# Optimization experiments

Measured on AMD Instinct MI355X. Metric: run time of the kernel, lower is better.

Reference implementation:

```python
import jax, jax.numpy as jnp
import numpy as np

N_NODES = 100000
N_EDGES = 1600000
IN_FEATS = 128
OUT_FEATS = 256
K = 32


def setup_inputs() -> dict:
    key = jax.random.key(0)
    ks = jax.random.split(key, 8)
    feat = jax.random.normal(ks[0], (N_NODES, IN_FEATS), dtype=jnp.float32)
    # MaxK sparsified activations: nonnegative values (post-ReLU top-k)
    topk_values = jax.random.uniform(ks[1], (N_NODES, K), dtype=jnp.float32)
    topk_indices = jax.random.randint(ks[2], (N_NODES, K), 0, IN_FEATS, dtype=jnp.int32)
    # CSR expanded to COO: sorted row ids emulate indptr ordering
    row = jnp.sort(jax.random.randint(ks[3], (N_EDGES,), 0, N_NODES, dtype=jnp.int32))
    col = jax.random.randint(ks[4], (N_EDGES,), 0, N_NODES, dtype=jnp.int32)
    # in-degrees clamped to min 1.0, as in set_graph_data
    deg = jax.ops.segment_sum(jnp.ones((N_EDGES,), jnp.float32), row, num_segments=N_NODES)
    degrees = jnp.maximum(deg, 1.0)
    gain = float(np.sqrt(2.0))  # calculate_gain('relu')
    bnd_n = gain * np.sqrt(6.0 / (IN_FEATS + OUT_FEATS))
    W_neigh = jax.random.uniform(ks[5], (IN_FEATS, OUT_FEATS), jnp.float32, -bnd_n, bnd_n)
    W_self = jax.random.uniform(ks[6], (IN_FEATS, OUT_FEATS), jnp.float32, -bnd_n, bnd_n)
    bnd_b = 1.0 / np.sqrt(IN_FEATS)
    b_self = jax.random.uniform(ks[7], (OUT_FEATS,), jnp.float32, -bnd_b, bnd_b)
    return {"feat": feat, "topk_values": topk_values, "topk_indices": topk_indices,
            "row": row, "col": col, "degrees": degrees,
            "W_neigh": W_neigh, "W_self": W_self, "b_self": b_self}


def reference(feat, topk_values, topk_indices, row, col, degrees, W_neigh, W_self, b_self):
    n = feat.shape[0]
    # Scatter top-k sparse features back to dense [N, in_feats]
    # (real top-k indices are unique per row, so add == set; add is deterministic)
    rows = jnp.arange(n, dtype=jnp.int32)[:, None]
    x_sparse = jnp.zeros((n, IN_FEATS), feat.dtype).at[rows, topk_indices].add(topk_values)
    # CSR SpMM with all-ones edge values + degree normalization (mean aggregation)
    gathered = x_sparse[col]                                  # [E, in_feats]
    agg = jax.ops.segment_sum(gathered, row, num_segments=n)  # [N, in_feats]
    agg = agg / degrees[:, None]
    # lin_before_mp is False (in_feats <= out_feats): linear after aggregation
    h_neigh = agg @ W_neigh                                    # [N, out_feats]
    rst = feat @ W_self + b_self + h_neigh
    return rst
```

## Files before the change

### kernel.cpp

```cpp
#include <hip/hip_runtime.h>
#include <stdint.h>

#define IN_FEATS 128
#define OUT_FEATS 256
#define TOPK 32
#define BM 128
#define BN 128
#define BK 64
#define KTOT 256

typedef float f32x4 __attribute__((ext_vector_type(4)));
typedef short bf16x8 __attribute__((ext_vector_type(8)));

__device__ __forceinline__ unsigned short f2bf(float x) {
    unsigned u = __float_as_uint(x);
    u += 0x7FFFu + ((u >> 16) & 1u);
    return (unsigned short)(u >> 16);
}

__device__ __forceinline__ void gload16(const void* g, void* l) {
    __builtin_amdgcn_global_load_lds(
        (const __attribute__((address_space(1))) unsigned*)g,
        (__attribute__((address_space(3))) unsigned*)l, 16, 0, 0);
}

__global__ __launch_bounds__(256) void k_scatter(
    const float* __restrict__ vals, const int* __restrict__ idxs,
    const float* __restrict__ feat,
    unsigned short* __restrict__ xsp, unsigned short* __restrict__ Acat,
    int n_nodes) {
    __shared__ float lds[4 * IN_FEATS];
    int t = threadIdx.x;
    int n0 = blockIdx.x * 4;
    lds[t] = 0.f;
    lds[t + 256] = 0.f;
    __syncthreads();
    if (t < 4 * TOPK) {
        int h = t >> 5;
        int k = t & 31;
        int n = n0 + h;
        if (n < n_nodes) {
            float v = vals[(size_t)n * TOPK + k];
            int ix = idxs[(size_t)n * TOPK + k] & 127;
            atomicAdd(&lds[h * IN_FEATS + ix], v);
        }
    }
    __syncthreads();
    int h2 = t >> 6;
    int f2 = (t & 63) * 2;
    int n = n0 + h2;
    if (n < n_nodes) {
        unsigned lo = f2bf(lds[h2 * IN_FEATS + f2]);
        unsigned hi = f2bf(lds[h2 * IN_FEATS + f2 + 1]);
        *(unsigned*)(xsp + (size_t)n * IN_FEATS + f2) = lo | (hi << 16);
        float2 fv = *(const float2*)(feat + (size_t)n * IN_FEATS + f2);
        unsigned pk = (unsigned)f2bf(fv.x) | ((unsigned)f2bf(fv.y) << 16);
        *(unsigned*)(Acat + (size_t)n * KTOT + IN_FEATS + f2) = pk;
    }
}

__global__ void k_weights(const float* __restrict__ Wn, const float* __restrict__ Ws,
                          unsigned short* __restrict__ WT) {
    int idx = blockIdx.x * 256 + threadIdx.x;
    int n = idx >> 8;
    int k = idx & 255;
    float v = (k < IN_FEATS) ? Wn[(size_t)k * OUT_FEATS + n]
                             : Ws[(size_t)(k - IN_FEATS) * OUT_FEATS + n];
    WT[idx] = f2bf(v);
}

__global__ void k_indptr(const int* __restrict__ row, int* __restrict__ indptr,
                         int n_nodes, int n_edges) {
    int e = blockIdx.x * 256 + threadIdx.x;
    if (e >= n_edges) return;
    int r = row[e];
    int rp = (e == 0) ? -1 : row[e - 1];
    for (int x = rp + 1; x <= r; ++x) indptr[x] = e;
    if (e == n_edges - 1)
        for (int x = r + 1; x <= n_nodes; ++x) indptr[x] = n_edges;
}

__global__ __launch_bounds__(256) void k_aggregate(
    const unsigned short* __restrict__ xsp,
    const int* __restrict__ indptr, const int* __restrict__ col,
    unsigned short* __restrict__ Acat, int n_nodes) {
    int t = threadIdx.x;
    int node = blockIdx.x * 4 + (t >> 6);
    if (node >= n_nodes) return;
    int lane = t & 63;
    int eg = lane >> 4, fi = lane & 15;
    int e0 = indptr[node], e1 = indptr[node + 1];

    float acc[8] = {0.f, 0.f, 0.f, 0.f, 0.f, 0.f, 0.f, 0.f};
    int elast = (e1 > e0) ? (e1 - 1) : e0;
    for (int base = e0; base < e1; base += 16) {
        float s[4];
        int c[4];
        uint4 u[4];
#pragma unroll
        for (int j = 0; j < 4; ++j) {
            int ee = base + j * 4 + eg;
            s[j] = (ee < e1) ? 1.f : 0.f;
            c[j] = col[ee < elast ? ee : elast];
        }
#pragma unroll
        for (int j = 0; j < 4; ++j)
            u[j] = *(const uint4*)(xsp + (size_t)c[j] * IN_FEATS + fi * 8);
#pragma unroll
        for (int j = 0; j < 4; ++j) {
            unsigned p[4] = {u[j].x, u[j].y, u[j].z, u[j].w};
#pragma unroll
            for (int i = 0; i < 4; ++i) {
                acc[2 * i]     = fmaf(s[j], __uint_as_float(p[i] << 16), acc[2 * i]);
                acc[2 * i + 1] = fmaf(s[j], __uint_as_float(p[i] & 0xFFFF0000u), acc[2 * i + 1]);
            }
        }
    }
#pragma unroll
    for (int i = 0; i < 8; ++i) {
        acc[i] += __shfl_down(acc[i], 16, 64);
        acc[i] += __shfl_down(acc[i], 32, 64);
    }
    if (eg == 0) {
        int cnt = e1 - e0;
        float inv = 1.0f / (float)(cnt > 0 ? cnt : 1);
        unsigned o[4];
#pragma unroll
        for (int i = 0; i < 4; ++i) {
            unsigned lo = f2bf(acc[2 * i] * inv);
            unsigned hi = f2bf(acc[2 * i + 1] * inv);
            o[i] = lo | (hi << 16);
        }
        *(uint4*)(Acat + (size_t)node * KTOT + fi * 8) = *(uint4*)&o[0];
    }
}

__global__ __launch_bounds__(256) void k_gemm(
    const unsigned short* __restrict__ Acat,
    const unsigned short* __restrict__ WT,
    const float* __restrict__ bias,
    float* __restrict__ out, int n_nodes) {
    __shared__ __align__(16) unsigned short Ash[BM * BK];
    __shared__ __align__(16) unsigned short Bsh[BN * BK];
    int t = threadIdx.x;
    int m0 = blockIdx.x * BM;
    int n0 = blockIdx.y * BN;
    int lane = t & 63;
    int w = t >> 6;
    int wr = w >> 1, wc = w & 1;
    int lrow = lane & 15, quad = lane >> 4;

    f32x4 acc[4][4];
#pragma unroll
    for (int i = 0; i < 4; ++i)
#pragma unroll
        for (int j = 0; j < 4; ++j)
            acc[i][j] = (f32x4){0.f, 0.f, 0.f, 0.f};

    for (int kk = 0; kk < KTOT; kk += BK) {
#pragma unroll
        for (int p = 0; p < 4; ++p) {
            int c = p * 256 + t;
            int row = c >> 3;
            int q = (c & 7) ^ (row & 7);
            int nodeA = m0 + row;
            if (nodeA >= n_nodes) nodeA = n_nodes - 1;
            gload16(Acat + (size_t)nodeA * KTOT + kk + q * 8, &Ash[(size_t)c * 8]);
            gload16(WT + (size_t)(n0 + row) * KTOT + kk + q * 8, &Bsh[(size_t)c * 8]);
        }
        __syncthreads();

#pragma unroll
        for (int ks = 0; ks < 2; ++ks) {
            bf16x8 af[4], bfr[4];
#pragma unroll
            for (int mi = 0; mi < 4; ++mi) {
                int r = wr * 64 + mi * 16 + lrow;
                int q = (ks * 4 + quad) ^ (r & 7);
                af[mi] = *(const bf16x8*)&Ash[(r * 8 + q) * 8];
            }
#pragma unroll
            for (int ni = 0; ni < 4; ++ni) {
                int r = wc * 64 + ni * 16 + lrow;
                int q = (ks * 4 + quad) ^ (r & 7);
                bfr[ni] = *(const bf16x8*)&Bsh[(r * 8 + q) * 8];
            }
#pragma unroll
            for (int mi = 0; mi < 4; ++mi)
#pragma unroll
                for (int ni = 0; ni < 4; ++ni)
                    acc[mi][ni] = __builtin_amdgcn_mfma_f32_16x16x32_bf16(
                        af[mi], bfr[ni], acc[mi][ni], 0, 0, 0);
        }
        __syncthreads();
    }

#pragma unroll
    for (int mi = 0; mi < 4; ++mi) {
        int gm = m0 + wr * 64 + mi * 16 + quad * 4;
#pragma unroll
        for (int ni = 0; ni < 4; ++ni) {
            int go = n0 + wc * 64 + ni * 16 + lrow;
            float b = bias[go];
#pragma unroll
            for (int r = 0; r < 4; ++r) {
                int node = gm + r;
                if (node < n_nodes)
                    out[(size_t)node * OUT_FEATS + go] = acc[mi][ni][r] + b;
            }
        }
    }
}

extern "C" void kernel_launch(void* const* d_in, const int* in_sizes, int n_in,
                              void* d_out, int out_size, void* d_ws, size_t ws_size,
                              hipStream_t stream) {
    const float* feat = (const float*)d_in[0];
    const float* tkv  = (const float*)d_in[1];
    const int*   tki  = (const int*)d_in[2];
    const int*   row  = (const int*)d_in[3];
    const int*   col  = (const int*)d_in[4];
    const float* Wn   = (const float*)d_in[6];
    const float* Ws   = (const float*)d_in[7];
    const float* bias = (const float*)d_in[8];
    float* out = (float*)d_out;

    int n_nodes = in_sizes[5];
    int n_edges = in_sizes[3];

    unsigned short* xsp  = (unsigned short*)d_ws;
    unsigned short* Acat = xsp + (size_t)n_nodes * IN_FEATS;
    unsigned short* WT   = Acat + (size_t)n_nodes * KTOT;
    int* indptr = (int*)(WT + (size_t)OUT_FEATS * KTOT);

    k_scatter<<<(n_nodes + 3) / 4, 256, 0, stream>>>(tkv, tki, feat, xsp, Acat, n_nodes);
    k_weights<<<256, 256, 0, stream>>>(Wn, Ws, WT);
    k_indptr<<<(n_edges + 255) / 256, 256, 0, stream>>>(row, indptr, n_nodes, n_edges);
    k_aggregate<<<(n_nodes + 3) / 4, 256, 0, stream>>>(xsp, indptr, col, Acat, n_nodes);
    dim3 g3((n_nodes + BM - 1) / BM, OUT_FEATS / BN);
    k_gemm<<<g3, 256, 0, stream>>>(Acat, WT, bias, out, n_nodes);
}
```

Measured before the change: 289.4 us.

## Drop indptr kernel via binary search and widen GEMM tile to full N

Removes the separate indptr-construction kernel. Each wavefront in the aggregate kernel now finds its CSR edge range with two binary searches over the sorted row array. The GEMM now uses 512-thread blocks that cover all 256 output columns, so each A tile is loaded once instead of twice. The cost is about 17 dependent global loads per node for the searches, plus higher LDS use and register pressure per GEMM block, which may lower occupancy.

```diff
diff --git a/kernel.cpp b/kernel.cpp
--- a/kernel.cpp
+++ b/kernel.cpp
@@ -5,7 +5,7 @@
 #define OUT_FEATS 256
 #define TOPK 32
 #define BM 128
-#define BN 128
+#define BN 256
 #define BK 64
 #define KTOT 256
 
@@ -69,27 +69,22 @@
     WT[idx] = f2bf(v);
 }
 
-__global__ void k_indptr(const int* __restrict__ row, int* __restrict__ indptr,
-                         int n_nodes, int n_edges) {
-    int e = blockIdx.x * 256 + threadIdx.x;
-    if (e >= n_edges) return;
-    int r = row[e];
-    int rp = (e == 0) ? -1 : row[e - 1];
-    for (int x = rp + 1; x <= r; ++x) indptr[x] = e;
-    if (e == n_edges - 1)
-        for (int x = r + 1; x <= n_nodes; ++x) indptr[x] = n_edges;
-}
-
 __global__ __launch_bounds__(256) void k_aggregate(
     const unsigned short* __restrict__ xsp,
-    const int* __restrict__ indptr, const int* __restrict__ col,
-    unsigned short* __restrict__ Acat, int n_nodes) {
+    const int* __restrict__ row, const int* __restrict__ col,
+    unsigned short* __restrict__ Acat, int n_nodes, int n_edges) {
     int t = threadIdx.x;
     int node = blockIdx.x * 4 + (t >> 6);
     if (node >= n_nodes) return;
     int lane = t & 63;
     int eg = lane >> 4, fi = lane & 15;
-    int e0 = indptr[node], e1 = indptr[node + 1];
+
+    int lo = 0, hi = n_edges;
+    while (lo < hi) { int mid = (lo + hi) >> 1; if (row[mid] < node) lo = mid + 1; else hi = mid; }
+    int e0 = lo;
+    hi = n_edges;
+    while (lo < hi) { int mid = (lo + hi) >> 1; if (row[mid] <= node) lo = mid + 1; else hi = mid; }
+    int e1 = lo;
 
     float acc[8] = {0.f, 0.f, 0.f, 0.f, 0.f, 0.f, 0.f, 0.f};
     int elast = (e1 > e0) ? (e1 - 1) : e0;
@@ -127,15 +122,15 @@
         unsigned o[4];
 #pragma unroll
         for (int i = 0; i < 4; ++i) {
-            unsigned lo = f2bf(acc[2 * i] * inv);
-            unsigned hi = f2bf(acc[2 * i + 1] * inv);
-            o[i] = lo | (hi << 16);
+            unsigned lo2 = f2bf(acc[2 * i] * inv);
+            unsigned hi2 = f2bf(acc[2 * i + 1] * inv);
+            o[i] = lo2 | (hi2 << 16);
         }
         *(uint4*)(Acat + (size_t)node * KTOT + fi * 8) = *(uint4*)&o[0];
     }
 }
 
-__global__ __launch_bounds__(256) void k_gemm(
+__global__ __launch_bounds__(512) void k_gemm(
     const unsigned short* __restrict__ Acat,
     const unsigned short* __restrict__ WT,
     const float* __restrict__ bias,
@@ -144,10 +139,9 @@
     __shared__ __align__(16) unsigned short Bsh[BN * BK];
     int t = threadIdx.x;
     int m0 = blockIdx.x * BM;
-    int n0 = blockIdx.y * BN;
     int lane = t & 63;
     int w = t >> 6;
-    int wr = w >> 1, wc = w & 1;
+    int wr = w >> 2, wc = w & 3;
     int lrow = lane & 15, quad = lane >> 4;
 
     f32x4 acc[4][4];
@@ -159,14 +153,20 @@
 
     for (int kk = 0; kk < KTOT; kk += BK) {
 #pragma unroll
-        for (int p = 0; p < 4; ++p) {
-            int c = p * 256 + t;
-            int row = c >> 3;
-            int q = (c & 7) ^ (row & 7);
-            int nodeA = m0 + row;
+        for (int p = 0; p < 2; ++p) {
+            int c = p * 512 + t;
+            int rowi = c >> 3;
+            int q = (c & 7) ^ (rowi & 7);
+            int nodeA = m0 + rowi;
             if (nodeA >= n_nodes) nodeA = n_nodes - 1;
             gload16(Acat + (size_t)nodeA * KTOT + kk + q * 8, &Ash[(size_t)c * 8]);
-            gload16(WT + (size_t)(n0 + row) * KTOT + kk + q * 8, &Bsh[(size_t)c * 8]);
+        }
+#pragma unroll
+        for (int p = 0; p < 4; ++p) {
+            int c = p * 512 + t;
+            int rowi = c >> 3;
+            int q = (c & 7) ^ (rowi & 7);
+            gload16(WT + (size_t)rowi * KTOT + kk + q * 8, &Bsh[(size_t)c * 8]);
         }
         __syncthreads();
 
@@ -200,7 +200,7 @@
         int gm = m0 + wr * 64 + mi * 16 + quad * 4;
 #pragma unroll
         for (int ni = 0; ni < 4; ++ni) {
-            int go = n0 + wc * 64 + ni * 16 + lrow;
+            int go = wc * 64 + ni * 16 + lrow;
             float b = bias[go];
 #pragma unroll
             for (int r = 0; r < 4; ++r) {
@@ -231,12 +231,9 @@
     unsigned short* xsp  = (unsigned short*)d_ws;
     unsigned short* Acat = xsp + (size_t)n_nodes * IN_FEATS;
     unsigned short* WT   = Acat + (size_t)n_nodes * KTOT;
-    int* indptr = (int*)(WT + (size_t)OUT_FEATS * KTOT);
 
     k_scatter<<<(n_nodes + 3) / 4, 256, 0, stream>>>(tkv, tki, feat, xsp, Acat, n_nodes);
     k_weights<<<256, 256, 0, stream>>>(Wn, Ws, WT);
-    k_indptr<<<(n_edges + 255) / 256, 256, 0, stream>>>(row, indptr, n_nodes, n_edges);
-    k_aggregate<<<(n_nodes + 3) / 4, 256, 0, stream>>>(xsp, indptr, col, Acat, n_nodes);
-    dim3 g3((n_nodes + BM - 1) / BM, OUT_FEATS / BN);
-    k_gemm<<<g3, 256, 0, stream>>>(Acat, WT, bias, out, n_nodes);
-}
+    k_aggregate<<<(n_nodes + 3) / 4, 256, 0, stream>>>(xsp, row, col, Acat, n_nodes, n_edges);
+    k_gemm<<<(n_nodes + BM - 1) / BM, 512, 0, stream>>>(Acat, WT, bias, out, n_nodes);
+}
```

After: 430.3 us. +48.7%, slower.
